# Optimization experiments

Measured on AMD Instinct MI355X. Metric: run time of the kernel, lower is better.

The kernel has to match this reference:

```python
import jax, jax.numpy as jnp
import numpy as np

S, N, C, E, L = 4, 50000, 256, 800000, 3
EPS = 1e-5  # nn.LayerNorm default eps


def setup_inputs() -> dict:
    key = jax.random.key(0)
    ks = jax.random.split(key, 10)
    sc = 1.0 / np.sqrt(C)
    x = jax.random.normal(ks[0], (S, N, C), jnp.float32)
    edge_index = jax.random.randint(ks[1], (S, 2, E), 0, N, dtype=jnp.int32)
    edge_weight = jax.random.uniform(ks[2], (S, E), jnp.float32)
    W_gcn = jax.random.uniform(ks[3], (L, C, C), jnp.float32, -sc, sc)
    b_gcn = jnp.zeros((L, C), jnp.float32)
    ln_scale = jnp.ones((L, C), jnp.float32)
    ln_bias = jnp.zeros((L, C), jnp.float32)
    w_ih = jax.random.uniform(ks[4], (3 * C, C), jnp.float32, -sc, sc)
    w_hh = jax.random.uniform(ks[5], (3 * C, C), jnp.float32, -sc, sc)
    b_ih = jax.random.uniform(ks[6], (3 * C,), jnp.float32, -sc, sc)
    b_hh = jax.random.uniform(ks[7], (3 * C,), jnp.float32, -sc, sc)
    return dict(x=x, edge_index=edge_index, edge_weight=edge_weight,
                W_gcn=W_gcn, b_gcn=b_gcn, ln_scale=ln_scale, ln_bias=ln_bias,
                w_ih=w_ih, w_hh=w_hh, b_ih=b_ih, b_hh=b_hh)


def _gcn_conv(h, row, col, ew, W, b):
    """PyG GCNConv: out = D^{-1/2} (A + I) D^{-1/2} (h W) + b, edge weights ew."""
    h = h @ W  # [N, C]
    loop = jnp.arange(N, dtype=row.dtype)
    row = jnp.concatenate([row, loop])
    col = jnp.concatenate([col, loop])
    ew = jnp.concatenate([ew, jnp.ones((N,), ew.dtype)])
    deg = jax.ops.segment_sum(ew, col, num_segments=N)  # in-degree at targets
    dinv = jnp.where(deg > 0, jax.lax.rsqrt(jnp.maximum(deg, EPS * 0 + 1e-12)), 0.0)
    norm = dinv[row] * ew * dinv[col]  # [E+N]
    msg = h[row] * norm[:, None]       # gather from sources
    return jax.ops.segment_sum(msg, col, num_segments=N) + b


def _layernorm(h, scale, bias):
    mu = jnp.mean(h, axis=-1, keepdims=True)
    var = jnp.mean(jnp.square(h - mu), axis=-1, keepdims=True)
    return (h - mu) * jax.lax.rsqrt(var + EPS) * scale + bias


def _snapshot(x, ei, ew, W_gcn, b_gcn, ln_scale, ln_bias):
    h = x
    row, col = ei[0], ei[1]
    for l in range(L):
        h = _gcn_conv(h, row, col, ew, W_gcn[l], b_gcn[l])
        h = _layernorm(h, ln_scale[l], ln_bias[l])
        h = jax.nn.relu(h)  # dropout is identity in eval mode
    return h


def _gru_last(seq, w_ih, w_hh, b_ih, b_hh):
    """seq: [S, N, C] -> final hidden [N, C] (torch single-layer GRU)."""
    def step(h, x_t):
        gi = x_t @ w_ih.T + b_ih
        gh = h @ w_hh.T + b_hh
        i_r, i_z, i_n = jnp.split(gi, 3, axis=-1)
        h_r, h_z, h_n = jnp.split(gh, 3, axis=-1)
        r = jax.nn.sigmoid(i_r + h_r)
        z = jax.nn.sigmoid(i_z + h_z)
        n = jnp.tanh(i_n + r * h_n)
        return (1.0 - z) * n + z * h, None
    h0 = jnp.zeros(seq.shape[1:], seq.dtype)
    h_last, _ = jax.lax.scan(step, h0, seq)
    return h_last


def reference(x, edge_index, edge_weight, W_gcn, b_gcn, ln_scale, ln_bias,
              w_ih, w_hh, b_ih, b_hh):
    feats = jax.vmap(lambda xs, eis, ews: _snapshot(xs, eis, ews, W_gcn, b_gcn, ln_scale, ln_bias))(
        x, edge_index, edge_weight)  # [S, N, C]
    return _gru_last(feats, w_ih, w_hh, b_ih, b_hh)  # [N, C]
```

## Files before the change

kernel.cpp:

```cpp
#include <hip/hip_runtime.h>
#include <cmath>

#define S_ 4
#define N_ 50000
#define C_ 256
#define E_ 800000
#define L_ 3
#define EPS_ 1e-5f
#define CAP_ 64

typedef __attribute__((ext_vector_type(8))) short bf16x8;
typedef __attribute__((ext_vector_type(4))) float f32x4;

__device__ __forceinline__ float bf2f(unsigned short s) {
  return __uint_as_float(((unsigned)s) << 16);
}
__device__ __forceinline__ unsigned short f2bf(float f) {
  unsigned u = __float_as_uint(f);
  return (unsigned short)((u + 0x7fffu + ((u >> 16) & 1u)) >> 16);
}

__device__ __forceinline__ void gload_lds16(const void* g, void* l) {
  __builtin_amdgcn_global_load_lds(
      (const __attribute__((address_space(1))) unsigned int*)g,
      (__attribute__((address_space(3))) unsigned int*)l, 16, 0, 0);
}

__device__ __forceinline__ void swz_block(int id, int nbx, int nby, int& bmi, int& bni) {
  const int NB8 = nby * 8;
  int fullb = (nbx >> 3) * NB8;
  if (id < fullb) {
    int g = id / NB8, pp = id - g * NB8;
    bmi = g * 8 + (pp & 7);
    bni = pp >> 3;
  } else {
    int rem = nbx & 7;
    int idp = id - fullb;
    bmi = (nbx & ~7) + idp % rem;
    bni = idp / rem;
  }
}

__global__ __launch_bounds__(256) void gemm_bf16_kernel(
    const unsigned short* __restrict__ A, const unsigned short* __restrict__ Bt,
    unsigned short* __restrict__ Cout, int M, int Nn, int K, int nby)
{
  __shared__ alignas(16) unsigned short As[2][128 * 32];
  __shared__ alignas(16) unsigned short Bs[2][128 * 32];
  const int tid = threadIdx.x;
  const int lane = tid & 63;
  const int wid = tid >> 6;
  const int wr = wid >> 1, wc = wid & 1;
  int bmi, bni;
  swz_block(blockIdx.x, gridDim.x / nby, nby, bmi, bni);
  const int bm = bmi * 128, bn = bni * 128;
  const int l15 = lane & 15, l4 = lane >> 4;

  f32x4 acc[4][4] = {};

  int offA[4], offB[4];
  #pragma unroll
  for (int mi = 0; mi < 4; ++mi) {
    int ra = wr * 64 + mi * 16 + l15;
    offA[mi] = ra * 32 + ((l4 ^ ((ra >> 1) & 3)) << 3);
    int rb = wc * 64 + mi * 16 + l15;
    offB[mi] = rb * 32 + ((l4 ^ ((rb >> 1) & 3)) << 3);
  }
  const int rs = tid >> 2;
  const int gs = tid & 3;

  auto stage = [&](int buf, int k0) {
    #pragma unroll
    for (int t2 = 0; t2 < 2; ++t2) {
      int r = rs + t2 * 64;
      int q = gs ^ ((r >> 1) & 3);
      int arow = bm + r; if (arow >= M) arow = M - 1;
      gload_lds16(&A[(size_t)arow * K + k0 + q * 8], &As[buf][(t2 * 256 + tid) * 8]);
      int brow = bn + r;
      gload_lds16(&Bt[(size_t)brow * K + k0 + q * 8], &Bs[buf][(t2 * 256 + tid) * 8]);
    }
  };

  const int nt = K >> 5;
  stage(0, 0);
  asm volatile("s_waitcnt vmcnt(0)" ::: "memory");
  __syncthreads();

  int cur = 0;
  for (int t = 0; t < nt; ++t) {
    if (t + 1 < nt) stage(cur ^ 1, (t + 1) * 32);

    bf16x8 af[4], bfr[4];
    #pragma unroll
    for (int mi = 0; mi < 4; ++mi) af[mi] = *(const bf16x8*)&As[cur][offA[mi]];
    #pragma unroll
    for (int ni = 0; ni < 4; ++ni) bfr[ni] = *(const bf16x8*)&Bs[cur][offB[ni]];
    #pragma unroll
    for (int mi = 0; mi < 4; ++mi)
      #pragma unroll
      for (int ni = 0; ni < 4; ++ni)
        acc[mi][ni] = __builtin_amdgcn_mfma_f32_16x16x32_bf16(
            af[mi], bfr[ni], acc[mi][ni], 0, 0, 0);

    asm volatile("s_waitcnt vmcnt(0)" ::: "memory");
    __syncthreads();
    cur ^= 1;
  }

  #pragma unroll
  for (int mi = 0; mi < 4; ++mi) {
    int rowb = bm + wr * 64 + mi * 16 + l4 * 4;
    #pragma unroll
    for (int ni = 0; ni < 4; ++ni) {
      int col = bn + wc * 64 + ni * 16 + l15;
      #pragma unroll
      for (int r = 0; r < 4; ++r) {
        int row = rowb + r;
        if (row < M) Cout[(size_t)row * Nn + col] = f2bf(acc[mi][ni][r]);
      }
    }
  }
}

__global__ __launch_bounds__(256) void gru_fused_kernel(
    const unsigned short* __restrict__ feat,
    const unsigned short* __restrict__ hq_in,
    const unsigned short* __restrict__ Wp_ih,
    const unsigned short* __restrict__ Wp_hh,
    const float* __restrict__ b_ih, const float* __restrict__ b_hh,
    unsigned short* __restrict__ hq_out, float* __restrict__ hout,
    int first, int M)
{
  __shared__ alignas(16) unsigned short As[2][128 * 32];
  __shared__ alignas(16) unsigned short Bs[2][96 * 32];
  const int tid = threadIdx.x;
  const int lane = tid & 63;
  const int wv = tid >> 6;
  const int l15 = lane & 15, l4 = lane >> 4;

  int bmi, bni;
  swz_block(blockIdx.x, gridDim.x / 8, 8, bmi, bni);
  const int bm = bmi * 128;
  const int c0 = bni * 32;
  const int brow0 = bni * 96;

  f32x4 acc_i[2][6] = {};
  f32x4 acc_h[2][6] = {};

  int offA[2], offB[6];
  #pragma unroll
  for (int mi = 0; mi < 2; ++mi) {
    int ra = wv * 32 + mi * 16 + l15;
    offA[mi] = ra * 32 + ((l4 ^ ((ra >> 1) & 3)) << 3);
  }
  #pragma unroll
  for (int ni = 0; ni < 6; ++ni) {
    int rb = ni * 16 + l15;
    offB[ni] = rb * 32 + ((l4 ^ ((rb >> 1) & 3)) << 3);
  }

  const int nt = first ? 8 : 16;

  auto stage = [&](int buf, int t) {
    int k0 = (t & 7) * 32;
    const unsigned short* Ap = (t < 8) ? feat : hq_in;
    const unsigned short* Bp = (t < 8) ? Wp_ih : Wp_hh;
    #pragma unroll
    for (int t2 = 0; t2 < 2; ++t2) {
      int slot = t2 * 256 + tid;
      int r = slot >> 2;
      int q = (slot & 3) ^ ((r >> 1) & 3);
      int arow = bm + r; if (arow >= M) arow = M - 1;
      gload_lds16(&Ap[(size_t)arow * 256 + k0 + q * 8], &As[buf][slot * 8]);
    }
    {
      int slot = tid;
      int r = slot >> 2;
      int q = (slot & 3) ^ ((r >> 1) & 3);
      gload_lds16(&Bp[(size_t)(brow0 + r) * 256 + k0 + q * 8], &Bs[buf][slot * 8]);
    }
    if (tid < 128) {
      int slot = 256 + tid;
      int r = slot >> 2;
      int q = (slot & 3) ^ ((r >> 1) & 3);
      gload_lds16(&Bp[(size_t)(brow0 + r) * 256 + k0 + q * 8], &Bs[buf][slot * 8]);
    }
  };

  stage(0, 0);
  asm volatile("s_waitcnt vmcnt(0)" ::: "memory");
  __syncthreads();

  int cur = 0;
  for (int t = 0; t < nt; ++t) {
    if (t + 1 < nt) stage(cur ^ 1, t + 1);

    bf16x8 af[2], bfr[6];
    #pragma unroll
    for (int mi = 0; mi < 2; ++mi) af[mi] = *(const bf16x8*)&As[cur][offA[mi]];
    #pragma unroll
    for (int ni = 0; ni < 6; ++ni) bfr[ni] = *(const bf16x8*)&Bs[cur][offB[ni]];
    if (t < 8) {
      #pragma unroll
      for (int mi = 0; mi < 2; ++mi)
        #pragma unroll
        for (int ni = 0; ni < 6; ++ni)
          acc_i[mi][ni] = __builtin_amdgcn_mfma_f32_16x16x32_bf16(
              af[mi], bfr[ni], acc_i[mi][ni], 0, 0, 0);
    } else {
      #pragma unroll
      for (int mi = 0; mi < 2; ++mi)
        #pragma unroll
        for (int ni = 0; ni < 6; ++ni)
          acc_h[mi][ni] = __builtin_amdgcn_mfma_f32_16x16x32_bf16(
              af[mi], bfr[ni], acc_h[mi][ni], 0, 0, 0);
    }

    asm volatile("s_waitcnt vmcnt(0)" ::: "memory");
    __syncthreads();
    cur ^= 1;
  }

  #pragma unroll
  for (int cni = 0; cni < 2; ++cni) {
    int c = c0 + cni * 16 + l15;
    float bir = b_ih[c], biz = b_ih[256 + c], bin = b_ih[512 + c];
    float bhr = b_hh[c], bhz = b_hh[256 + c], bhn = b_hh[512 + c];
    #pragma unroll
    for (int mi = 0; mi < 2; ++mi) {
      int rowb = bm + wv * 32 + mi * 16 + l4 * 4;
      #pragma unroll
      for (int rr = 0; rr < 4; ++rr) {
        int row = rowb + rr;
        if (row < M) {
          float gir = acc_i[mi][0 + cni][rr] + bir;
          float ghr = acc_h[mi][0 + cni][rr] + bhr;
          float giz = acc_i[mi][2 + cni][rr] + biz;
          float ghz = acc_h[mi][2 + cni][rr] + bhz;
          float gin = acc_i[mi][4 + cni][rr] + bin;
          float ghn = acc_h[mi][4 + cni][rr] + bhn;
          float rg = 1.f / (1.f + expf(-(gir + ghr)));
          float zg = 1.f / (1.f + expf(-(giz + ghz)));
          float ng = tanhf(gin + rg * ghn);
          float hp = first ? 0.f : bf2f(hq_in[(size_t)row * 256 + c]);
          float hv = (1.f - zg) * ng + zg * hp;
          if (hq_out) hq_out[(size_t)row * 256 + c] = f2bf(hv);
          if (hout) hout[(size_t)row * 256 + c] = hv;
        }
      }
    }
  }
}

__global__ void prep_wgcn_kernel(const float* __restrict__ W, unsigned short* __restrict__ Wt) {
  int i = blockIdx.x * blockDim.x + threadIdx.x;
  if (i < L_ * C_ * C_) {
    int l = i / (C_ * C_);
    int rem = i - l * C_ * C_;
    int nn = rem >> 8, k = rem & 255;
    Wt[i] = f2bf(W[l * C_ * C_ + k * C_ + nn]);
  }
}
__global__ void prep_wp_kernel(const float* __restrict__ W, unsigned short* __restrict__ Wp) {
  int d = blockIdx.x * blockDim.x + threadIdx.x;
  if (d < 768 * 256) {
    int jrow = d >> 8, k = d & 255;
    int chunk = jrow / 96, j = jrow - chunk * 96;
    int g = j >> 5, dc = j & 31;
    int srow = g * 256 + chunk * 32 + dc;
    Wp[d] = f2bf(W[srow * 256 + k]);
  }
}
__global__ void quant_kernel(const float* __restrict__ in, unsigned short* __restrict__ out, int n4) {
  int i = blockIdx.x * blockDim.x + threadIdx.x;
  if (i < n4) {
    float4 v = ((const float4*)in)[i];
    ushort4 q;
    q.x = f2bf(v.x); q.y = f2bf(v.y); q.z = f2bf(v.z); q.w = f2bf(v.w);
    *(ushort4*)&out[i * 4] = q;
  }
}

__global__ void scatter_fill_kernel(const int* __restrict__ edge_idx,
                                    const float* __restrict__ edge_w,
                                    unsigned long long* __restrict__ recs,
                                    int* __restrict__ cnt_g) {
  int e = blockIdx.x * blockDim.x + threadIdx.x;
  if (e < S_ * E_) {
    int s = e / E_;
    int ee = e - s * E_;
    int r = edge_idx[(size_t)s * 2 * E_ + ee];
    int c = edge_idx[(size_t)s * 2 * E_ + E_ + ee];
    float w = edge_w[(size_t)s * E_ + ee];
    int ng = s * N_ + c;
    int pos = atomicAdd(&cnt_g[ng], 1);
    if (pos < CAP_) {
      recs[((size_t)ng << 6) + pos] =
          ((unsigned long long)__float_as_uint(w) << 32) | (unsigned int)r;
    }
  }
}

__global__ __launch_bounds__(256) void deg_dinv_kernel(
    const unsigned long long* __restrict__ recs, const int* __restrict__ cnt_g,
    float* __restrict__ dinv_g) {
  const int lane = threadIdx.x & 63, wv = threadIdx.x >> 6;
  const int ng = blockIdx.x * 4 + wv;
  int cnt = min(cnt_g[ng], CAP_);
  float w = 0.f;
  if (lane < cnt)
    w = __uint_as_float((unsigned int)(recs[((size_t)ng << 6) + lane] >> 32));
  #pragma unroll
  for (int off = 32; off > 0; off >>= 1) w += __shfl_xor(w, off);
  if (lane == 0) dinv_g[ng] = rsqrtf(w + 1.0f);
}

__global__ void normify_kernel(const unsigned long long* __restrict__ recs,
                               const int* __restrict__ cnt_g,
                               const float* __restrict__ dinv_g,
                               unsigned int* __restrict__ src_norm) {
  int idx = blockIdx.x * blockDim.x + threadIdx.x;
  if (idx < S_ * N_ * CAP_) {
    int ng = idx >> 6, slot = idx & 63;
    int cnt = min(cnt_g[ng], CAP_);
    if (slot < cnt) {
      unsigned long long rec = recs[idx];
      int src = (int)(unsigned int)rec & 0xFFFF;
      float w = __uint_as_float((unsigned int)(rec >> 32));
      int s = ng / N_;
      float nrm = dinv_g[s * N_ + src] * w * dinv_g[ng];
      src_norm[idx] = (unsigned int)src | ((unsigned int)f2bf(nrm) << 16);
    }
  }
}

__global__ __launch_bounds__(256) void spmm_ln_relu_kernel(
    const unsigned short* __restrict__ hW_all, const int* __restrict__ cnt_g,
    const unsigned int* __restrict__ src_norm, const float* __restrict__ dinv_g,
    const float* __restrict__ bgcn, const float* __restrict__ lnsc,
    const float* __restrict__ lnbi, unsigned short* __restrict__ out)
{
  const int tid = threadIdx.x;
  const int lane = tid & 63, wv = tid >> 6;
  const int n_g = blockIdx.x * 4 + wv;
  const int s = n_g / N_;
  const int n = n_g - s * N_;
  const int c4 = lane << 2;
  const unsigned short* hW = hW_all + ((size_t)s * N_ << 8);

  const int cnt = min(cnt_g[n_g], CAP_);
  unsigned int rec = (lane < cnt) ? src_norm[((size_t)n_g << 6) + lane] : 0u;

  float a0, a1, a2, a3;
  {
    float dv = dinv_g[n_g];
    float w = dv * dv;
    ushort4 u = *(const ushort4*)&hW[((size_t)n << 8) + c4];
    a0 = w * bf2f(u.x); a1 = w * bf2f(u.y); a2 = w * bf2f(u.z); a3 = w * bf2f(u.w);
  }
  int j = 0;
  for (; j + 3 < cnt; j += 4) {
    unsigned int r0 = __shfl((int)rec, j + 0);
    unsigned int r1 = __shfl((int)rec, j + 1);
    unsigned int r2 = __shfl((int)rec, j + 2);
    unsigned int r3 = __shfl((int)rec, j + 3);
    ushort4 u0 = *(const ushort4*)&hW[((size_t)(r0 & 0xFFFFu) << 8) + c4];
    ushort4 u1 = *(const ushort4*)&hW[((size_t)(r1 & 0xFFFFu) << 8) + c4];
    ushort4 u2 = *(const ushort4*)&hW[((size_t)(r2 & 0xFFFFu) << 8) + c4];
    ushort4 u3 = *(const ushort4*)&hW[((size_t)(r3 & 0xFFFFu) << 8) + c4];
    float n0 = bf2f((unsigned short)(r0 >> 16));
    float n1 = bf2f((unsigned short)(r1 >> 16));
    float n2 = bf2f((unsigned short)(r2 >> 16));
    float n3 = bf2f((unsigned short)(r3 >> 16));
    a0 = fmaf(n0, bf2f(u0.x), a0); a1 = fmaf(n0, bf2f(u0.y), a1);
    a2 = fmaf(n0, bf2f(u0.z), a2); a3 = fmaf(n0, bf2f(u0.w), a3);
    a0 = fmaf(n1, bf2f(u1.x), a0); a1 = fmaf(n1, bf2f(u1.y), a1);
    a2 = fmaf(n1, bf2f(u1.z), a2); a3 = fmaf(n1, bf2f(u1.w), a3);
    a0 = fmaf(n2, bf2f(u2.x), a0); a1 = fmaf(n2, bf2f(u2.y), a1);
    a2 = fmaf(n2, bf2f(u2.z), a2); a3 = fmaf(n2, bf2f(u2.w), a3);
    a0 = fmaf(n3, bf2f(u3.x), a0); a1 = fmaf(n3, bf2f(u3.y), a1);
    a2 = fmaf(n3, bf2f(u3.z), a2); a3 = fmaf(n3, bf2f(u3.w), a3);
  }
  for (; j < cnt; ++j) {
    unsigned int r0 = __shfl((int)rec, j);
    ushort4 u0 = *(const ushort4*)&hW[((size_t)(r0 & 0xFFFFu) << 8) + c4];
    float n0 = bf2f((unsigned short)(r0 >> 16));
    a0 = fmaf(n0, bf2f(u0.x), a0); a1 = fmaf(n0, bf2f(u0.y), a1);
    a2 = fmaf(n0, bf2f(u0.z), a2); a3 = fmaf(n0, bf2f(u0.w), a3);
  }

  float4 bg = *(const float4*)&bgcn[c4];
  float v0 = a0 + bg.x, v1 = a1 + bg.y, v2 = a2 + bg.z, v3 = a3 + bg.w;
  float s1 = (v0 + v1) + (v2 + v3);
  float s2 = (v0 * v0 + v1 * v1) + (v2 * v2 + v3 * v3);
  #pragma unroll
  for (int off = 32; off > 0; off >>= 1) {
    s1 += __shfl_xor(s1, off);
    s2 += __shfl_xor(s2, off);
  }
  float mu = s1 * (1.0f / C_);
  float var = s2 * (1.0f / C_) - mu * mu;
  float inv = rsqrtf(var + EPS_);
  float4 sc = *(const float4*)&lnsc[c4];
  float4 bi = *(const float4*)&lnbi[c4];
  ushort4 o;
  o.x = f2bf(fmaxf((v0 - mu) * inv * sc.x + bi.x, 0.f));
  o.y = f2bf(fmaxf((v1 - mu) * inv * sc.y + bi.y, 0.f));
  o.z = f2bf(fmaxf((v2 - mu) * inv * sc.z + bi.z, 0.f));
  o.w = f2bf(fmaxf((v3 - mu) * inv * sc.w + bi.w, 0.f));
  *(ushort4*)&out[((size_t)n_g << 8) + c4] = o;
}

extern "C" void kernel_launch(void* const* d_in, const int* in_sizes, int n_in,
                              void* d_out, int out_size, void* d_ws, size_t ws_size,
                              hipStream_t stream) {
  const float* x        = (const float*)d_in[0];
  const int*   edge_idx = (const int*)d_in[1];
  const float* edge_w   = (const float*)d_in[2];
  const float* W_gcn    = (const float*)d_in[3];
  const float* b_gcn    = (const float*)d_in[4];
  const float* ln_scale = (const float*)d_in[5];
  const float* ln_bias  = (const float*)d_in[6];
  const float* w_ih     = (const float*)d_in[7];
  const float* w_hh     = (const float*)d_in[8];
  const float* b_ih     = (const float*)d_in[9];
  const float* b_hh     = (const float*)d_in[10];
  float* h_out = (float*)d_out;

  char* p = (char*)d_ws;
  auto carve = [&](size_t bytes) -> void* {
    void* r = (void*)p;
    p += (bytes + 255) & ~(size_t)255;
    return r;
  };
  unsigned long long* recs = (unsigned long long*)carve((size_t)S_ * N_ * CAP_ * 8);
  unsigned int* src_norm = (unsigned int*)carve((size_t)S_ * N_ * CAP_ * 4);
  int*   cnt_g       = (int*)carve((size_t)S_ * N_ * 4);
  float* dinv_g      = (float*)carve((size_t)S_ * N_ * 4);
  unsigned short* wt_gcn = (unsigned short*)carve((size_t)L_ * C_ * C_ * 2);
  unsigned short* wp_ih  = (unsigned short*)carve((size_t)768 * C_ * 2);
  unsigned short* wp_hh  = (unsigned short*)carve((size_t)768 * C_ * 2);
  unsigned short* xq_all = (unsigned short*)carve((size_t)S_ * N_ * C_ * 2);
  unsigned short* hW_all = (unsigned short*)carve((size_t)S_ * N_ * C_ * 2);
  unsigned short* fA_all = (unsigned short*)carve((size_t)S_ * N_ * C_ * 2);
  unsigned short* hq0    = (unsigned short*)carve((size_t)N_ * C_ * 2);
  unsigned short* hq1    = (unsigned short*)carve((size_t)N_ * C_ * 2);

  const int TB = 256;

  hipMemsetAsync(cnt_g, 0, (size_t)S_ * N_ * 4, stream);

  prep_wgcn_kernel<<<(L_ * C_ * C_ + TB - 1) / TB, TB, 0, stream>>>(W_gcn, wt_gcn);
  prep_wp_kernel<<<(768 * C_ + TB - 1) / TB, TB, 0, stream>>>(w_ih, wp_ih);
  prep_wp_kernel<<<(768 * C_ + TB - 1) / TB, TB, 0, stream>>>(w_hh, wp_hh);

  quant_kernel<<<((size_t)S_ * N_ * C_ / 4 + TB - 1) / TB, TB, 0, stream>>>(
      x, xq_all, S_ * N_ * C_ / 4);

  scatter_fill_kernel<<<(S_ * E_ + TB - 1) / TB, TB, 0, stream>>>(
      edge_idx, edge_w, recs, cnt_g);
  deg_dinv_kernel<<<S_ * N_ / 4, TB, 0, stream>>>(recs, cnt_g, dinv_g);
  normify_kernel<<<(S_ * N_ * CAP_ + TB - 1) / TB, TB, 0, stream>>>(
      recs, cnt_g, dinv_g, src_norm);

  const int M_all = S_ * N_;
  const int nbx = (M_all + 127) / 128;
  {
    const unsigned short* hin = xq_all;
    for (int l = 0; l < L_; ++l) {
      unsigned short* fout = (l == 1) ? xq_all : fA_all;
      gemm_bf16_kernel<<<nbx * (C_ / 128), 256, 0, stream>>>(
          hin, wt_gcn + (size_t)l * C_ * C_, hW_all, M_all, C_, C_, C_ / 128);
      spmm_ln_relu_kernel<<<M_all / 4, 256, 0, stream>>>(
          hW_all, cnt_g, src_norm, dinv_g, b_gcn + l * C_,
          ln_scale + l * C_, ln_bias + l * C_, fout);
      hin = fout;
    }
  }
  const unsigned short* feat_all = fA_all;

  const int gnb = ((N_ + 127) / 128) * 8;
  unsigned short* hq_cur = hq0;
  unsigned short* hq_nxt = hq1;
  for (int s = 0; s < S_; ++s) {
    bool last = (s == S_ - 1);
    gru_fused_kernel<<<gnb, 256, 0, stream>>>(
        feat_all + (size_t)s * N_ * C_,
        hq_cur,
        wp_ih, wp_hh, b_ih, b_hh,
        last ? nullptr : hq_nxt,
        last ? h_out : nullptr,
        (s == 0) ? 1 : 0, N_);
    unsigned short* t = hq_cur; hq_cur = hq_nxt; hq_nxt = t;
  }
}
```

Baseline: 1.645 ms.

## Fuse fp32 input quantization into first GEMM and vectorize GEMM/GRU epilogues

The first-layer GEMM now reads fp32 x directly, converts it to bf16 in registers and writes it to LDS, so the separate quant kernel and its bf16 copy of x go away. The MFMA operand order is swapped so each lane holds 4 consecutive output columns, which lets the GEMM and GRU epilogues issue vectorized ushort4/float4 stores and bias loads. The three weight-prep kernels are merged into one launch. The fp32 A path adds register pressure and an LDS write through VGPRs instead of direct global-to-LDS loads, which may slow the first GEMM.

```diff
diff --git a/kernel.cpp b/kernel.cpp
--- a/kernel.cpp
+++ b/kernel.cpp
@@ -41,8 +41,10 @@
   }
 }
 
+template<bool AF32>
 __global__ __launch_bounds__(256) void gemm_bf16_kernel(
-    const unsigned short* __restrict__ A, const unsigned short* __restrict__ Bt,
+    const unsigned short* __restrict__ A, const float* __restrict__ Af,
+    const unsigned short* __restrict__ Bt,
     unsigned short* __restrict__ Cout, int M, int Nn, int K, int nby)
 {
   __shared__ alignas(16) unsigned short As[2][128 * 32];
@@ -69,26 +71,71 @@
   const int rs = tid >> 2;
   const int gs = tid & 3;
 
-  auto stage = [&](int buf, int k0) {
+  float4 fa[2][2];
+
+  auto loadA_f32 = [&](int k0) {
+    #pragma unroll
+    for (int t2 = 0; t2 < 2; ++t2) {
+      int r = rs + t2 * 64;
+      int q = gs ^ ((r >> 1) & 3);
+      int arow = bm + r; if (arow >= M) arow = M - 1;
+      const float* srcp = &Af[(size_t)arow * K + k0 + q * 8];
+      fa[t2][0] = *(const float4*)srcp;
+      fa[t2][1] = *(const float4*)(srcp + 4);
+    }
+  };
+  auto writeA_f32 = [&](int buf) {
+    #pragma unroll
+    for (int t2 = 0; t2 < 2; ++t2) {
+      int slot = t2 * 256 + tid;
+      union { unsigned short us[8]; bf16x8 v; } u;
+      const float* f = (const float*)&fa[t2][0];
+      #pragma unroll
+      for (int j = 0; j < 8; ++j) u.us[j] = f2bf(f[j]);
+      *(bf16x8*)&As[buf][slot * 8] = u.v;
+    }
+  };
+  auto stageA_bf = [&](int buf, int k0) {
     #pragma unroll
     for (int t2 = 0; t2 < 2; ++t2) {
       int r = rs + t2 * 64;
       int q = gs ^ ((r >> 1) & 3);
       int arow = bm + r; if (arow >= M) arow = M - 1;
       gload_lds16(&A[(size_t)arow * K + k0 + q * 8], &As[buf][(t2 * 256 + tid) * 8]);
-      int brow = bn + r;
-      gload_lds16(&Bt[(size_t)brow * K + k0 + q * 8], &Bs[buf][(t2 * 256 + tid) * 8]);
     }
   };
+  auto stageB = [&](int buf, int k0) {
+    #pragma unroll
+    for (int t2 = 0; t2 < 2; ++t2) {
+      int r = rs + t2 * 64;
+      int q = gs ^ ((r >> 1) & 3);
+      gload_lds16(&Bt[(size_t)(bn + r) * K + k0 + q * 8], &Bs[buf][(t2 * 256 + tid) * 8]);
+    }
+  };
 
   const int nt = K >> 5;
-  stage(0, 0);
+  if constexpr (AF32) {
+    loadA_f32(0);
+    stageB(0, 0);
+    writeA_f32(0);
+  } else {
+    stageA_bf(0, 0);
+    stageB(0, 0);
+  }
   asm volatile("s_waitcnt vmcnt(0)" ::: "memory");
   __syncthreads();
 
   int cur = 0;
   for (int t = 0; t < nt; ++t) {
-    if (t + 1 < nt) stage(cur ^ 1, (t + 1) * 32);
+    if (t + 1 < nt) {
+      if constexpr (AF32) {
+        loadA_f32((t + 1) * 32);
+        stageB(cur ^ 1, (t + 1) * 32);
+      } else {
+        stageA_bf(cur ^ 1, (t + 1) * 32);
+        stageB(cur ^ 1, (t + 1) * 32);
+      }
+    }
 
     bf16x8 af[4], bfr[4];
     #pragma unroll
@@ -100,8 +147,11 @@
       #pragma unroll
       for (int ni = 0; ni < 4; ++ni)
         acc[mi][ni] = __builtin_amdgcn_mfma_f32_16x16x32_bf16(
-            af[mi], bfr[ni], acc[mi][ni], 0, 0, 0);
-
+            bfr[ni], af[mi], acc[mi][ni], 0, 0, 0);
+
+    if constexpr (AF32) {
+      if (t + 1 < nt) writeA_f32(cur ^ 1);
+    }
     asm volatile("s_waitcnt vmcnt(0)" ::: "memory");
     __syncthreads();
     cur ^= 1;
@@ -109,14 +159,17 @@
 
   #pragma unroll
   for (int mi = 0; mi < 4; ++mi) {
-    int rowb = bm + wr * 64 + mi * 16 + l4 * 4;
-    #pragma unroll
-    for (int ni = 0; ni < 4; ++ni) {
-      int col = bn + wc * 64 + ni * 16 + l15;
+    int row = bm + wr * 64 + mi * 16 + l15;
+    if (row < M) {
       #pragma unroll
-      for (int r = 0; r < 4; ++r) {
-        int row = rowb + r;
-        if (row < M) Cout[(size_t)row * Nn + col] = f2bf(acc[mi][ni][r]);
+      for (int ni = 0; ni < 4; ++ni) {
+        int colb = bn + wc * 64 + ni * 16 + l4 * 4;
+        ushort4 o;
+        o.x = f2bf(acc[mi][ni][0]);
+        o.y = f2bf(acc[mi][ni][1]);
+        o.z = f2bf(acc[mi][ni][2]);
+        o.w = f2bf(acc[mi][ni][3]);
+        *(ushort4*)&Cout[(size_t)row * Nn + colb] = o;
       }
     }
   }
@@ -206,14 +259,14 @@
         #pragma unroll
         for (int ni = 0; ni < 6; ++ni)
           acc_i[mi][ni] = __builtin_amdgcn_mfma_f32_16x16x32_bf16(
-              af[mi], bfr[ni], acc_i[mi][ni], 0, 0, 0);
+              bfr[ni], af[mi], acc_i[mi][ni], 0, 0, 0);
     } else {
       #pragma unroll
       for (int mi = 0; mi < 2; ++mi)
         #pragma unroll
         for (int ni = 0; ni < 6; ++ni)
           acc_h[mi][ni] = __builtin_amdgcn_mfma_f32_16x16x32_bf16(
-              af[mi], bfr[ni], acc_h[mi][ni], 0, 0, 0);
+              bfr[ni], af[mi], acc_h[mi][ni], 0, 0, 0);
     }
 
     asm volatile("s_waitcnt vmcnt(0)" ::: "memory");
@@ -222,62 +275,79 @@
   }
 
   #pragma unroll
-  for (int cni = 0; cni < 2; ++cni) {
-    int c = c0 + cni * 16 + l15;
-    float bir = b_ih[c], biz = b_ih[256 + c], bin = b_ih[512 + c];
-    float bhr = b_hh[c], bhz = b_hh[256 + c], bhn = b_hh[512 + c];
-    #pragma unroll
-    for (int mi = 0; mi < 2; ++mi) {
-      int rowb = bm + wv * 32 + mi * 16 + l4 * 4;
+  for (int mi = 0; mi < 2; ++mi) {
+    int row = bm + wv * 32 + mi * 16 + l15;
+    if (row < M) {
       #pragma unroll
-      for (int rr = 0; rr < 4; ++rr) {
-        int row = rowb + rr;
-        if (row < M) {
-          float gir = acc_i[mi][0 + cni][rr] + bir;
-          float ghr = acc_h[mi][0 + cni][rr] + bhr;
-          float giz = acc_i[mi][2 + cni][rr] + biz;
-          float ghz = acc_h[mi][2 + cni][rr] + bhz;
-          float gin = acc_i[mi][4 + cni][rr] + bin;
-          float ghn = acc_h[mi][4 + cni][rr] + bhn;
+      for (int cni = 0; cni < 2; ++cni) {
+        int dc = cni * 16 + l4 * 4;
+        int c = c0 + dc;
+        float4 bir = *(const float4*)&b_ih[c];
+        float4 biz = *(const float4*)&b_ih[256 + c];
+        float4 bin = *(const float4*)&b_ih[512 + c];
+        float4 bhr = *(const float4*)&b_hh[c];
+        float4 bhz = *(const float4*)&b_hh[256 + c];
+        float4 bhn = *(const float4*)&b_hh[512 + c];
+        float hpv[4] = {0.f, 0.f, 0.f, 0.f};
+        if (!first) {
+          ushort4 hp = *(const ushort4*)&hq_in[(size_t)row * 256 + c];
+          hpv[0] = bf2f(hp.x); hpv[1] = bf2f(hp.y);
+          hpv[2] = bf2f(hp.z); hpv[3] = bf2f(hp.w);
+        }
+        const float* pbir = (const float*)&bir; const float* pbiz = (const float*)&biz;
+        const float* pbin = (const float*)&bin; const float* pbhr = (const float*)&bhr;
+        const float* pbhz = (const float*)&bhz; const float* pbhn = (const float*)&bhn;
+        float hv[4];
+        #pragma unroll
+        for (int rr = 0; rr < 4; ++rr) {
+          float gir = acc_i[mi][0 + cni][rr] + pbir[rr];
+          float giz = acc_i[mi][2 + cni][rr] + pbiz[rr];
+          float gin = acc_i[mi][4 + cni][rr] + pbin[rr];
+          float ghr = (first ? 0.f : acc_h[mi][0 + cni][rr]) + pbhr[rr];
+          float ghz = (first ? 0.f : acc_h[mi][2 + cni][rr]) + pbhz[rr];
+          float ghn = (first ? 0.f : acc_h[mi][4 + cni][rr]) + pbhn[rr];
           float rg = 1.f / (1.f + expf(-(gir + ghr)));
           float zg = 1.f / (1.f + expf(-(giz + ghz)));
           float ng = tanhf(gin + rg * ghn);
-          float hp = first ? 0.f : bf2f(hq_in[(size_t)row * 256 + c]);
-          float hv = (1.f - zg) * ng + zg * hp;
-          if (hq_out) hq_out[(size_t)row * 256 + c] = f2bf(hv);
-          if (hout) hout[(size_t)row * 256 + c] = hv;
+          hv[rr] = (1.f - zg) * ng + zg * hpv[rr];
+        }
+        if (hq_out) {
+          ushort4 o;
+          o.x = f2bf(hv[0]); o.y = f2bf(hv[1]); o.z = f2bf(hv[2]); o.w = f2bf(hv[3]);
+          *(ushort4*)&hq_out[(size_t)row * 256 + c] = o;
+        }
+        if (hout) {
+          float4 o = make_float4(hv[0], hv[1], hv[2], hv[3]);
+          *(float4*)&hout[(size_t)row * 256 + c] = o;
         }
       }
     }
   }
 }
 
-__global__ void prep_wgcn_kernel(const float* __restrict__ W, unsigned short* __restrict__ Wt) {
+__global__ void prep_weights_kernel(const float* __restrict__ W_gcn,
+                                    const float* __restrict__ w_ih,
+                                    const float* __restrict__ w_hh,
+                                    unsigned short* __restrict__ wt_gcn,
+                                    unsigned short* __restrict__ wp_ih,
+                                    unsigned short* __restrict__ wp_hh) {
   int i = blockIdx.x * blockDim.x + threadIdx.x;
-  if (i < L_ * C_ * C_) {
+  const int LCC = L_ * C_ * C_, WSZ = 768 * C_;
+  if (i < LCC) {
     int l = i / (C_ * C_);
     int rem = i - l * C_ * C_;
     int nn = rem >> 8, k = rem & 255;
-    Wt[i] = f2bf(W[l * C_ * C_ + k * C_ + nn]);
-  }
-}
-__global__ void prep_wp_kernel(const float* __restrict__ W, unsigned short* __restrict__ Wp) {
-  int d = blockIdx.x * blockDim.x + threadIdx.x;
-  if (d < 768 * 256) {
+    wt_gcn[i] = f2bf(W_gcn[l * C_ * C_ + k * C_ + nn]);
+  } else if (i < LCC + 2 * WSZ) {
+    int j = i - LCC;
+    int which = j / WSZ;
+    int d = j - which * WSZ;
     int jrow = d >> 8, k = d & 255;
-    int chunk = jrow / 96, j = jrow - chunk * 96;
-    int g = j >> 5, dc = j & 31;
+    int chunk = jrow / 96, jj = jrow - chunk * 96;
+    int g = jj >> 5, dc = jj & 31;
     int srow = g * 256 + chunk * 32 + dc;
-    Wp[d] = f2bf(W[srow * 256 + k]);
-  }
-}
-__global__ void quant_kernel(const float* __restrict__ in, unsigned short* __restrict__ out, int n4) {
-  int i = blockIdx.x * blockDim.x + threadIdx.x;
-  if (i < n4) {
-    float4 v = ((const float4*)in)[i];
-    ushort4 q;
-    q.x = f2bf(v.x); q.y = f2bf(v.y); q.z = f2bf(v.z); q.w = f2bf(v.w);
-    *(ushort4*)&out[i * 4] = q;
+    float v = which ? w_hh[srow * 256 + k] : w_ih[srow * 256 + k];
+    (which ? wp_hh : wp_ih)[d] = f2bf(v);
   }
 }
 
@@ -440,9 +510,9 @@
   unsigned short* wt_gcn = (unsigned short*)carve((size_t)L_ * C_ * C_ * 2);
   unsigned short* wp_ih  = (unsigned short*)carve((size_t)768 * C_ * 2);
   unsigned short* wp_hh  = (unsigned short*)carve((size_t)768 * C_ * 2);
-  unsigned short* xq_all = (unsigned short*)carve((size_t)S_ * N_ * C_ * 2);
   unsigned short* hW_all = (unsigned short*)carve((size_t)S_ * N_ * C_ * 2);
   unsigned short* fA_all = (unsigned short*)carve((size_t)S_ * N_ * C_ * 2);
+  unsigned short* fB_all = (unsigned short*)carve((size_t)S_ * N_ * C_ * 2);
   unsigned short* hq0    = (unsigned short*)carve((size_t)N_ * C_ * 2);
   unsigned short* hq1    = (unsigned short*)carve((size_t)N_ * C_ * 2);
 
@@ -450,12 +520,9 @@
 
   hipMemsetAsync(cnt_g, 0, (size_t)S_ * N_ * 4, stream);
 
-  prep_wgcn_kernel<<<(L_ * C_ * C_ + TB - 1) / TB, TB, 0, stream>>>(W_gcn, wt_gcn);
-  prep_wp_kernel<<<(768 * C_ + TB - 1) / TB, TB, 0, stream>>>(w_ih, wp_ih);
-  prep_wp_kernel<<<(768 * C_ + TB - 1) / TB, TB, 0, stream>>>(w_hh, wp_hh);
-
-  quant_kernel<<<((size_t)S_ * N_ * C_ / 4 + TB - 1) / TB, TB, 0, stream>>>(
-      x, xq_all, S_ * N_ * C_ / 4);
+  const int PREP_N = L_ * C_ * C_ + 2 * 768 * C_;
+  prep_weights_kernel<<<(PREP_N + TB - 1) / TB, TB, 0, stream>>>(
+      W_gcn, w_ih, w_hh, wt_gcn, wp_ih, wp_hh);
 
   scatter_fill_kernel<<<(S_ * E_ + TB - 1) / TB, TB, 0, stream>>>(
       edge_idx, edge_w, recs, cnt_g);
@@ -466,15 +533,20 @@
   const int M_all = S_ * N_;
   const int nbx = (M_all + 127) / 128;
   {
-    const unsigned short* hin = xq_all;
+    unsigned short* louts[3] = {fA_all, fB_all, fA_all};
+    const unsigned short* hin = nullptr;
     for (int l = 0; l < L_; ++l) {
-      unsigned short* fout = (l == 1) ? xq_all : fA_all;
-      gemm_bf16_kernel<<<nbx * (C_ / 128), 256, 0, stream>>>(
-          hin, wt_gcn + (size_t)l * C_ * C_, hW_all, M_all, C_, C_, C_ / 128);
+      if (l == 0) {
+        gemm_bf16_kernel<true><<<nbx * (C_ / 128), 256, 0, stream>>>(
+            nullptr, x, wt_gcn, hW_all, M_all, C_, C_, C_ / 128);
+      } else {
+        gemm_bf16_kernel<false><<<nbx * (C_ / 128), 256, 0, stream>>>(
+            hin, nullptr, wt_gcn + (size_t)l * C_ * C_, hW_all, M_all, C_, C_, C_ / 128);
+      }
       spmm_ln_relu_kernel<<<M_all / 4, 256, 0, stream>>>(
           hW_all, cnt_g, src_norm, dinv_g, b_gcn + l * C_,
-          ln_scale + l * C_, ln_bias + l * C_, fout);
-      hin = fout;
+          ln_scale + l * C_, ln_bias + l * C_, louts[l]);
+      hin = louts[l];
     }
   }
   const unsigned short* feat_all = fA_all;
```

Measured after the change: 1.563 ms. 5.0% less time.
